# Kernel tuning notes

Hardware: AMD Instinct MI355X
Metric: run time of the kernel (lower is better)

The kernel has to match this reference:

```python
import jax, jax.numpy as jnp
import numpy as np

B, D_IN, D_OUT = 16384, 512, 64
H1, H2, GH = 64, 32, 32
E_SH, G, E_G = 2, 2, 2
LN_EPS = 1e-5


def _expert(v, w1, b1, w2, b2, w3, b3, gamma, beta):
    # MLP(input->64->32->D_OUT, Swish on hiddens, linear final) + LayerNorm(D_OUT)
    h = jax.nn.silu(v @ w1 + b1)
    h = jax.nn.silu(h @ w2 + b2)
    o = h @ w3 + b3
    mu = jnp.mean(o, axis=-1, keepdims=True)
    var = jnp.mean((o - mu) ** 2, axis=-1, keepdims=True)
    return gamma * (o - mu) * jax.lax.rsqrt(var + LN_EPS) + beta


def _gate(v, w1, b1, w2, b2):
    # MLP(input->32->E, Swish hidden, linear final) then softmax over experts
    h = jax.nn.silu(v @ w1 + b1)
    return jax.nn.softmax(h @ w2 + b2, axis=-1)


def setup_inputs() -> dict:
    key = jax.random.key(0)
    ks = iter(jax.random.split(key, 16))

    def rn(shape, scale=0.02):
        return jax.random.normal(next(ks), shape, dtype=jnp.float32) * scale

    return {
        "v": jax.random.normal(next(ks), (B, D_IN), dtype=jnp.float32),
        # shared experts (stacked over expert axis E_SH)
        "sw1": rn((E_SH, D_IN, H1)), "sb1": jnp.zeros((E_SH, H1), jnp.float32),
        "sw2": rn((E_SH, H1, H2)), "sb2": jnp.zeros((E_SH, H2), jnp.float32),
        "sw3": rn((E_SH, H2, D_OUT)), "sb3": jnp.zeros((E_SH, D_OUT), jnp.float32),
        "sgam": jnp.ones((E_SH, D_OUT), jnp.float32), "sbet": jnp.zeros((E_SH, D_OUT), jnp.float32),
        # shared gate
        "sgw1": rn((D_IN, GH)), "sgb1": jnp.zeros((GH,), jnp.float32),
        "sgw2": rn((GH, E_SH)), "sgb2": jnp.zeros((E_SH,), jnp.float32),
        # group experts (stacked over [G, E_G])
        "gw1": rn((G, E_G, D_IN, H1)), "gb1": jnp.zeros((G, E_G, H1), jnp.float32),
        "gw2": rn((G, E_G, H1, H2)), "gb2": jnp.zeros((G, E_G, H2), jnp.float32),
        "gw3": rn((G, E_G, H2, D_OUT)), "gb3": jnp.zeros((G, E_G, D_OUT), jnp.float32),
        "ggam": jnp.ones((G, E_G, D_OUT), jnp.float32), "gbet": jnp.zeros((G, E_G, D_OUT), jnp.float32),
        # group gates (stacked over G)
        "ggw1": rn((G, D_IN, GH)), "ggb1": jnp.zeros((G, GH), jnp.float32),
        "ggw2": rn((G, GH, E_G)), "ggb2": jnp.zeros((G, E_G), jnp.float32),
    }


def reference(v, sw1, sb1, sw2, sb2, sw3, sb3, sgam, sbet,
              sgw1, sgb1, sgw2, sgb2,
              gw1, gb1, gw2, gb2, gw3, gb3, ggam, gbet,
              ggw1, ggb1, ggw2, ggb2):
    expert_v = jax.vmap(_expert, in_axes=(None, 0, 0, 0, 0, 0, 0, 0, 0))
    # shared branch
    sh_outs = expert_v(v, sw1, sb1, sw2, sb2, sw3, sb3, sgam, sbet)   # [E, B, D]
    sh_w = _gate(v, sgw1, sgb1, sgw2, sgb2)                           # [B, E]
    z_shared = jnp.einsum('ebd,be->bd', sh_outs, sh_w)                # [B, D]
    # group branches (vmap over group axis G, inner vmap over experts)
    grp_expert = jax.vmap(expert_v, in_axes=(None, 0, 0, 0, 0, 0, 0, 0, 0))
    g_outs = grp_expert(v, gw1, gb1, gw2, gb2, gw3, gb3, ggam, gbet)  # [G, E, B, D]
    g_w = jax.vmap(_gate, in_axes=(None, 0, 0, 0, 0))(v, ggw1, ggb1, ggw2, ggb2)  # [G, B, E]
    z_groups = jnp.einsum('gebd,gbe->gbd', g_outs, g_w)               # [G, B, D]
    # stack (group_0, group_1, shared) -> [G+1, B, D]
    return jnp.concatenate([z_groups, z_shared[None]], axis=0)
```

## Files before the change

kernel.cpp:

```cpp
#include <hip/hip_runtime.h>

typedef short short8 __attribute__((ext_vector_type(8)));
typedef float f32x4 __attribute__((ext_vector_type(4)));

enum : unsigned {
  OFF_A   = 0u,
  OFF_B1  = 16777216u,
  OFF_B2  = 17268736u,
  OFF_B3  = 17293312u,
  OFF_b1  = 17317888u,
  OFF_b2  = 17319808u,
  OFF_b3  = 17320576u,
  OFF_gam = 17322112u,
  OFF_bet = 17323648u,
  OFF_gw2 = 17325184u,
  OFF_gb2 = 17325952u
};

__device__ __forceinline__ unsigned short f2bf(float x) {
  unsigned u = __builtin_bit_cast(unsigned, x);
  return (unsigned short)((u + 0x7fffu + ((u >> 16) & 1u)) >> 16);
}
__device__ __forceinline__ float bf2f(unsigned short b) {
  unsigned u = ((unsigned)b) << 16;
  return __builtin_bit_cast(float, u);
}
__device__ __forceinline__ float silu(float x) { return x / (1.f + __expf(-x)); }
__device__ __forceinline__ int fragk(int lane, int j) {
  return ((lane >> 4) << 2) + (j & 3) + ((j >> 2) << 4);
}

__global__ void pack_A(const float* __restrict__ v, unsigned char* __restrict__ ws) {
  int t = blockIdx.x * blockDim.x + threadIdx.x;
  int lane = t & 63, ks = (t >> 6) & 15, mtile = t >> 10;
  int row = mtile * 16 + (lane & 15);
  int k0  = ks * 32 + ((lane >> 4) << 2);
  const float* base = v + row * 512 + k0;
  float4 lo = *(const float4*)base;
  float4 hi = *(const float4*)(base + 16);
  short8 o;
  o[0] = (short)f2bf(lo.x); o[1] = (short)f2bf(lo.y);
  o[2] = (short)f2bf(lo.z); o[3] = (short)f2bf(lo.w);
  o[4] = (short)f2bf(hi.x); o[5] = (short)f2bf(hi.y);
  o[6] = (short)f2bf(hi.z); o[7] = (short)f2bf(hi.w);
  ((short8*)(ws + OFF_A))[t] = o;
}

__global__ void pack_W(
    const float* __restrict__ sw1, const float* __restrict__ sb1,
    const float* __restrict__ sw2, const float* __restrict__ sb2,
    const float* __restrict__ sw3, const float* __restrict__ sb3,
    const float* __restrict__ sgam, const float* __restrict__ sbet,
    const float* __restrict__ sgw1, const float* __restrict__ sgb1,
    const float* __restrict__ sgw2, const float* __restrict__ sgb2,
    const float* __restrict__ gw1, const float* __restrict__ gb1,
    const float* __restrict__ gw2, const float* __restrict__ gb2,
    const float* __restrict__ gw3, const float* __restrict__ gb3,
    const float* __restrict__ ggam, const float* __restrict__ gbet,
    const float* __restrict__ ggw1, const float* __restrict__ ggb1,
    const float* __restrict__ ggw2, const float* __restrict__ ggb2,
    unsigned char* __restrict__ ws) {
  int id = blockIdx.x * blockDim.x + threadIdx.x;

  if (id < 30720) {
    int lane = id & 63; int rest = id >> 6;
    int nt = rest % 10; int rk = rest / 10;
    int ks = rk & 15; int branch = rk >> 4;
    int col = nt * 16 + (lane & 15);
    short8 o;
#pragma unroll
    for (int j = 0; j < 8; ++j) {
      int k = ks * 32 + fragk(lane, j);
      float w;
      if (branch < 2) {
        if (col < 128) w = gw1[((branch * 2 + (col >> 6)) * 512 + k) * 64 + (col & 63)];
        else           w = ggw1[(branch * 512 + k) * 32 + (col - 128)];
      } else {
        if (col < 128) w = sw1[((col >> 6) * 512 + k) * 64 + (col & 63)];
        else           w = sgw1[k * 32 + (col - 128)];
      }
      o[j] = (short)f2bf(w);
    }
    ((short8*)(ws + OFF_B1))[id] = o;
    return;
  }
  id -= 30720;
  if (id < 1536) {
    int lane = id & 63; int rest = id >> 6;
    int nt = rest & 1, kk = (rest >> 1) & 1, eid = rest >> 2;
    int n = nt * 16 + (lane & 15);
    short8 o;
#pragma unroll
    for (int j = 0; j < 8; ++j) {
      int k = kk * 32 + fragk(lane, j);
      float w = (eid < 4) ? gw2[(eid * 64 + k) * 32 + n] : sw2[((eid - 4) * 64 + k) * 32 + n];
      o[j] = (short)f2bf(w);
    }
    ((short8*)(ws + OFF_B2))[id] = o;
    return;
  }
  id -= 1536;
  if (id < 1536) {
    int lane = id & 63; int rest = id >> 6;
    int nt = rest & 3, eid = rest >> 2;
    int n = nt * 16 + (lane & 15);
    short8 o;
#pragma unroll
    for (int j = 0; j < 8; ++j) {
      int k = fragk(lane, j);
      float w = (eid < 4) ? gw3[(eid * 32 + k) * 64 + n] : sw3[((eid - 4) * 32 + k) * 64 + n];
      o[j] = (short)f2bf(w);
    }
    ((short8*)(ws + OFF_B3))[id] = o;
    return;
  }
  id -= 1536;
  if (id < 480) {
    int branch = id / 160, col = id % 160;
    float w;
    if (col < 128) w = (branch < 2) ? gb1[(branch * 2 + (col >> 6)) * 64 + (col & 63)]
                                    : sb1[(col >> 6) * 64 + (col & 63)];
    else           w = (branch < 2) ? ggb1[branch * 32 + (col - 128)] : sgb1[col - 128];
    ((float*)(ws + OFF_b1))[id] = w;
    return;
  }
  id -= 480;
  if (id < 192) { ((float*)(ws + OFF_b2))[id] = (id < 128) ? gb2[id] : sb2[id - 128]; return; }
  id -= 192;
  if (id < 384) { ((float*)(ws + OFF_b3))[id] = (id < 256) ? gb3[id] : sb3[id - 256]; return; }
  id -= 384;
  if (id < 384) { ((float*)(ws + OFF_gam))[id] = (id < 256) ? ggam[id] : sgam[id - 256]; return; }
  id -= 384;
  if (id < 384) { ((float*)(ws + OFF_bet))[id] = (id < 256) ? gbet[id] : sbet[id - 256]; return; }
  id -= 384;
  if (id < 192) { int branch = id / 64; ((float*)(ws + OFF_gw2))[id] = (branch < 2) ? ggw2[id] : sgw2[id % 64]; return; }
  id -= 192;
  if (id < 6)  { ((float*)(ws + OFF_gb2))[id] = (id < 4) ? ggb2[id] : sgb2[id % 2]; return; }
}

__global__ __launch_bounds__(256) void home_main(const unsigned char* __restrict__ ws,
                                                 float* __restrict__ out) {
  const int lane = threadIdx.x & 63, wave = threadIdx.x >> 6;
  const int branch = blockIdx.y;
  const int mtile = blockIdx.x * 4 + wave;
  const int col16 = lane & 15, g4 = lane >> 4;

  const short8* Ap = (const short8*)(ws + OFF_A);
  const short8* B1 = (const short8*)(ws + OFF_B1);
  const short8* B2 = (const short8*)(ws + OFF_B2);
  const short8* B3 = (const short8*)(ws + OFF_B3);
  const float* b1c  = (const float*)(ws + OFF_b1) + branch * 160;
  const float* b2c  = (const float*)(ws + OFF_b2);
  const float* b3c  = (const float*)(ws + OFF_b3);
  const float* gamc = (const float*)(ws + OFF_gam);
  const float* betc = (const float*)(ws + OFF_bet);
  const float* gw2c = (const float*)(ws + OFF_gw2) + branch * 64;
  const float* gb2c = (const float*)(ws + OFF_gb2) + branch * 2;

  __shared__ unsigned short h1l[4][16][164];
  __shared__ unsigned short h2l[4][16][68];
  __shared__ float gatew[4][16][2];

  f32x4 acc[10];
#pragma unroll
  for (int nt = 0; nt < 10; ++nt) acc[nt] = (f32x4){0.f, 0.f, 0.f, 0.f};

#pragma unroll 2
  for (int ks = 0; ks < 16; ++ks) {
    short8 a = Ap[(mtile * 16 + ks) * 64 + lane];
#pragma unroll
    for (int nt = 0; nt < 10; ++nt) {
      short8 b = B1[((branch * 16 + ks) * 10 + nt) * 64 + lane];
      acc[nt] = __builtin_amdgcn_mfma_f32_16x16x32_bf16(a, b, acc[nt], 0, 0, 0);
    }
  }

#pragma unroll
  for (int nt = 0; nt < 10; ++nt) {
    int col = nt * 16 + col16;
    float bb = b1c[col];
#pragma unroll
    for (int r = 0; r < 4; ++r) {
      int row = (g4 << 2) + r;
      h1l[wave][row][col] = f2bf(silu(acc[nt][r] + bb));
    }
  }
  __syncthreads();

  {
    int rowg = (lane >> 1) & 15;
    int e = lane & 1;
    float logit = gb2c[e];
#pragma unroll 8
    for (int j = 0; j < 32; ++j)
      logit += bf2f(h1l[wave][rowg][128 + j]) * gw2c[j * 2 + e];
    float other = __shfl_xor(logit, 1, 64);
    float mx = fmaxf(logit, other);
    float a0 = __expf(logit - mx), a1 = __expf(other - mx);
    if (lane < 32) gatew[wave][rowg][e] = a0 / (a0 + a1);
  }

#pragma unroll
  for (int e2 = 0; e2 < 2; ++e2) {
    const int eid = (branch < 2) ? branch * 2 + e2 : 4 + e2;
    f32x4 a2[2];
    a2[0] = (f32x4){0.f, 0.f, 0.f, 0.f};
    a2[1] = (f32x4){0.f, 0.f, 0.f, 0.f};
#pragma unroll
    for (int kk = 0; kk < 2; ++kk) {
      const unsigned short* p = &h1l[wave][col16][e2 * 64 + kk * 32 + (g4 << 2)];
      union { short8 s; unsigned u[4]; } af;
      af.u[0] = *(const unsigned*)p;        af.u[1] = *(const unsigned*)(p + 2);
      af.u[2] = *(const unsigned*)(p + 16); af.u[3] = *(const unsigned*)(p + 18);
#pragma unroll
      for (int nt = 0; nt < 2; ++nt) {
        short8 b = B2[((eid * 2 + kk) * 2 + nt) * 64 + lane];
        a2[nt] = __builtin_amdgcn_mfma_f32_16x16x32_bf16(af.s, b, a2[nt], 0, 0, 0);
      }
    }
#pragma unroll
    for (int nt = 0; nt < 2; ++nt) {
      int c2 = nt * 16 + col16;
      float bb = b2c[eid * 32 + c2];
#pragma unroll
      for (int r = 0; r < 4; ++r) {
        int row = (g4 << 2) + r;
        h2l[wave][row][e2 * 32 + c2] = f2bf(silu(a2[nt][r] + bb));
      }
    }
  }
  __syncthreads();

  float z[4][4];
#pragma unroll
  for (int r = 0; r < 4; ++r)
#pragma unroll
    for (int nt = 0; nt < 4; ++nt) z[r][nt] = 0.f;

#pragma unroll
  for (int e2 = 0; e2 < 2; ++e2) {
    const int eid = (branch < 2) ? branch * 2 + e2 : 4 + e2;
    f32x4 a3[4];
#pragma unroll
    for (int nt = 0; nt < 4; ++nt) a3[nt] = (f32x4){0.f, 0.f, 0.f, 0.f};
    const unsigned short* p = &h2l[wave][col16][e2 * 32 + (g4 << 2)];
    union { short8 s; unsigned u[4]; } af;
    af.u[0] = *(const unsigned*)p;        af.u[1] = *(const unsigned*)(p + 2);
    af.u[2] = *(const unsigned*)(p + 16); af.u[3] = *(const unsigned*)(p + 18);
#pragma unroll
    for (int nt = 0; nt < 4; ++nt) {
      short8 b = B3[(eid * 4 + nt) * 64 + lane];
      a3[nt] = __builtin_amdgcn_mfma_f32_16x16x32_bf16(af.s, b, a3[nt], 0, 0, 0);
    }
#pragma unroll
    for (int r = 0; r < 4; ++r) {
      float o[4], s = 0.f, s2 = 0.f;
#pragma unroll
      for (int nt = 0; nt < 4; ++nt) {
        o[nt] = a3[nt][r] + b3c[eid * 64 + nt * 16 + col16];
        s += o[nt]; s2 += o[nt] * o[nt];
      }
#pragma unroll
      for (int m = 1; m < 16; m <<= 1) {
        s  += __shfl_xor(s, m, 64);
        s2 += __shfl_xor(s2, m, 64);
      }
      float mu  = s * 0.015625f;
      float var = s2 * 0.015625f - mu * mu;
      float inv = rsqrtf(var + 1e-5f);
      int row = (g4 << 2) + r;
      float wt = gatew[wave][row][e2];
#pragma unroll
      for (int nt = 0; nt < 4; ++nt) {
        int c = nt * 16 + col16;
        float ln = (o[nt] - mu) * inv * gamc[eid * 64 + c] + betc[eid * 64 + c];
        z[r][nt] += wt * ln;
      }
    }
  }

#pragma unroll
  for (int r = 0; r < 4; ++r) {
    int grow = mtile * 16 + (g4 << 2) + r;
#pragma unroll
    for (int nt = 0; nt < 4; ++nt)
      out[(branch * 16384 + grow) * 64 + nt * 16 + col16] = z[r][nt];
  }
}

extern "C" void kernel_launch(void* const* d_in, const int* in_sizes, int n_in,
                              void* d_out, int out_size, void* d_ws, size_t ws_size,
                              hipStream_t stream) {
  const float* v    = (const float*)d_in[0];
  const float* sw1  = (const float*)d_in[1];
  const float* sb1  = (const float*)d_in[2];
  const float* sw2  = (const float*)d_in[3];
  const float* sb2  = (const float*)d_in[4];
  const float* sw3  = (const float*)d_in[5];
  const float* sb3  = (const float*)d_in[6];
  const float* sgam = (const float*)d_in[7];
  const float* sbet = (const float*)d_in[8];
  const float* sgw1 = (const float*)d_in[9];
  const float* sgb1 = (const float*)d_in[10];
  const float* sgw2 = (const float*)d_in[11];
  const float* sgb2 = (const float*)d_in[12];
  const float* gw1  = (const float*)d_in[13];
  const float* gb1  = (const float*)d_in[14];
  const float* gw2  = (const float*)d_in[15];
  const float* gb2  = (const float*)d_in[16];
  const float* gw3  = (const float*)d_in[17];
  const float* gb3  = (const float*)d_in[18];
  const float* ggam = (const float*)d_in[19];
  const float* gbet = (const float*)d_in[20];
  const float* ggw1 = (const float*)d_in[21];
  const float* ggb1 = (const float*)d_in[22];
  const float* ggw2 = (const float*)d_in[23];
  const float* ggb2 = (const float*)d_in[24];
  unsigned char* ws = (unsigned char*)d_ws;
  float* out = (float*)d_out;

  pack_A<<<dim3(4096), dim3(256), 0, stream>>>(v, ws);
  pack_W<<<dim3(140), dim3(256), 0, stream>>>(
      sw1, sb1, sw2, sb2, sw3, sb3, sgam, sbet, sgw1, sgb1, sgw2, sgb2,
      gw1, gb1, gw2, gb2, gw3, gb3, ggam, gbet, ggw1, ggb1, ggw2, ggb2, ws);
  home_main<<<dim3(256, 3), dim3(256), 0, stream>>>(ws, out);
}
```

Baseline: 158.3 us.

## Fuse input bf16 packing into main kernel and stage B1 via double-buffered LDS

```diff
diff --git a/kernel.cpp b/kernel.cpp
--- a/kernel.cpp
+++ b/kernel.cpp
@@ -4,17 +4,16 @@
 typedef float f32x4 __attribute__((ext_vector_type(4)));
 
 enum : unsigned {
-  OFF_A   = 0u,
-  OFF_B1  = 16777216u,
-  OFF_B2  = 17268736u,
-  OFF_B3  = 17293312u,
-  OFF_b1  = 17317888u,
-  OFF_b2  = 17319808u,
-  OFF_b3  = 17320576u,
-  OFF_gam = 17322112u,
-  OFF_bet = 17323648u,
-  OFF_gw2 = 17325184u,
-  OFF_gb2 = 17325952u
+  OFF_B1  = 0u,
+  OFF_B2  = 491520u,
+  OFF_B3  = 516096u,
+  OFF_b1  = 540672u,
+  OFF_b2  = 542592u,
+  OFF_b3  = 543360u,
+  OFF_gam = 544896u,
+  OFF_bet = 546432u,
+  OFF_gw2 = 547968u,
+  OFF_gb2 = 548736u
 };
 
 __device__ __forceinline__ unsigned short f2bf(float x) {
@@ -28,22 +27,6 @@
 __device__ __forceinline__ float silu(float x) { return x / (1.f + __expf(-x)); }
 __device__ __forceinline__ int fragk(int lane, int j) {
   return ((lane >> 4) << 2) + (j & 3) + ((j >> 2) << 4);
-}
-
-__global__ void pack_A(const float* __restrict__ v, unsigned char* __restrict__ ws) {
-  int t = blockIdx.x * blockDim.x + threadIdx.x;
-  int lane = t & 63, ks = (t >> 6) & 15, mtile = t >> 10;
-  int row = mtile * 16 + (lane & 15);
-  int k0  = ks * 32 + ((lane >> 4) << 2);
-  const float* base = v + row * 512 + k0;
-  float4 lo = *(const float4*)base;
-  float4 hi = *(const float4*)(base + 16);
-  short8 o;
-  o[0] = (short)f2bf(lo.x); o[1] = (short)f2bf(lo.y);
-  o[2] = (short)f2bf(lo.z); o[3] = (short)f2bf(lo.w);
-  o[4] = (short)f2bf(hi.x); o[5] = (short)f2bf(hi.y);
-  o[6] = (short)f2bf(hi.z); o[7] = (short)f2bf(hi.w);
-  ((short8*)(ws + OFF_A))[t] = o;
 }
 
 __global__ void pack_W(
@@ -138,15 +121,16 @@
   if (id < 6)  { ((float*)(ws + OFF_gb2))[id] = (id < 4) ? ggb2[id] : sgb2[id % 2]; return; }
 }
 
-__global__ __launch_bounds__(256) void home_main(const unsigned char* __restrict__ ws,
-                                                 float* __restrict__ out) {
-  const int lane = threadIdx.x & 63, wave = threadIdx.x >> 6;
+__global__ __launch_bounds__(256) void fused_main(const float* __restrict__ v,
+                                                  const unsigned char* __restrict__ ws,
+                                                  float* __restrict__ out) {
+  const int tid  = threadIdx.x;
+  const int lane = tid & 63, wave = tid >> 6;
   const int branch = blockIdx.y;
   const int mtile = blockIdx.x * 4 + wave;
   const int col16 = lane & 15, g4 = lane >> 4;
 
-  const short8* Ap = (const short8*)(ws + OFF_A);
-  const short8* B1 = (const short8*)(ws + OFF_B1);
+  const short8* B1 = (const short8*)(ws + OFF_B1) + branch * 16 * 640;
   const short8* B2 = (const short8*)(ws + OFF_B2);
   const short8* B3 = (const short8*)(ws + OFF_B3);
   const float* b1c  = (const float*)(ws + OFF_b1) + branch * 160;
@@ -157,21 +141,52 @@
   const float* gw2c = (const float*)(ws + OFF_gw2) + branch * 64;
   const float* gb2c = (const float*)(ws + OFF_gb2) + branch * 2;
 
+  __shared__ short8 b1s[2][640];
   __shared__ unsigned short h1l[4][16][164];
   __shared__ unsigned short h2l[4][16][68];
   __shared__ float gatew[4][16][2];
 
+  {
+    short8 r0 = B1[tid];
+    short8 r1 = B1[tid + 256];
+    b1s[0][tid] = r0;
+    b1s[0][tid + 256] = r1;
+    if (tid < 128) b1s[0][tid + 512] = B1[tid + 512];
+  }
+
   f32x4 acc[10];
 #pragma unroll
   for (int nt = 0; nt < 10; ++nt) acc[nt] = (f32x4){0.f, 0.f, 0.f, 0.f};
 
-#pragma unroll 2
+  const float* vrow = v + (mtile * 16 + col16) * 512 + (g4 << 2);
+
   for (int ks = 0; ks < 16; ++ks) {
-    short8 a = Ap[(mtile * 16 + ks) * 64 + lane];
+    const int cur = ks & 1;
+    short8 s0, s1, s2;
+    if (ks < 15) {
+      const short8* src = B1 + (ks + 1) * 640;
+      s0 = src[tid];
+      s1 = src[tid + 256];
+      if (tid < 128) s2 = src[tid + 512];
+    }
+    __syncthreads();
+    float4 lo = *(const float4*)(vrow + ks * 32);
+    float4 hi = *(const float4*)(vrow + ks * 32 + 16);
+    short8 a;
+    a[0] = (short)f2bf(lo.x); a[1] = (short)f2bf(lo.y);
+    a[2] = (short)f2bf(lo.z); a[3] = (short)f2bf(lo.w);
+    a[4] = (short)f2bf(hi.x); a[5] = (short)f2bf(hi.y);
+    a[6] = (short)f2bf(hi.z); a[7] = (short)f2bf(hi.w);
 #pragma unroll
     for (int nt = 0; nt < 10; ++nt) {
-      short8 b = B1[((branch * 16 + ks) * 10 + nt) * 64 + lane];
+      short8 b = b1s[cur][nt * 64 + lane];
       acc[nt] = __builtin_amdgcn_mfma_f32_16x16x32_bf16(a, b, acc[nt], 0, 0, 0);
+    }
+    if (ks < 15) {
+      const int nxt = cur ^ 1;
+      b1s[nxt][tid] = s0;
+      b1s[nxt][tid + 256] = s1;
+      if (tid < 128) b1s[nxt][tid + 512] = s2;
     }
   }
 
@@ -319,9 +334,8 @@
   unsigned char* ws = (unsigned char*)d_ws;
   float* out = (float*)d_out;
 
-  pack_A<<<dim3(4096), dim3(256), 0, stream>>>(v, ws);
   pack_W<<<dim3(140), dim3(256), 0, stream>>>(
       sw1, sb1, sw2, sb2, sw3, sb3, sgam, sbet, sgw1, sgb1, sgw2, sgb2,
       gw1, gb1, gw2, gb2, gw3, gb3, ggam, gbet, ggw1, ggb1, ggw2, ggb2, ws);
-  home_main<<<dim3(256, 3), dim3(256), 0, stream>>>(ws, out);
-}
+  fused_main<<<dim3(256, 3), dim3(256), 0, stream>>>(v, ws, out);
+}
```

New measurement: 143.6 us. 9.3% less time.
